# Kernel optimization log

Hardware: AMD Instinct MI355X
Metric: run time of the kernel (lower is better)

## Reference

```python
import jax, jax.numpy as jnp
import numpy as np
import math

# dims
B, L, D = 2, 2048, 1024          # batch, seq len, embedding_dim
HID, ATT, H = 1024, 512, 8       # linear_hidden_dim, attention_dim, num_heads
DQK, DUV = ATT // H, HID // H    # 64, 128
NBUCK = 64                       # time_num_buckets
MAX_SPAN = 86400 * 90            # max_time_span
EPS = 1e-6
OUT_DIM = 2 * HID + 2 * ATT      # uvqk output dim = 3072


def _time_boundaries():
    # RelativeAttentionBiasModule._build_boundaries: pure log buckets
    steps = NBUCK - 1
    log_part = np.exp(np.linspace(0.0, math.log(MAX_SPAN), steps))
    b = np.unique(np.floor(np.clip(log_part, 1, None)).astype(np.int64)).astype(np.float32)
    return jnp.asarray(b)

_BOUNDARIES = _time_boundaries()  # len <= 63, indices < NBUCK


def setup_inputs() -> dict:
    key = jax.random.key(0)
    ks = jax.random.split(key, 8)
    x = jax.random.normal(ks[0], (B, L, D), dtype=jnp.float32)
    timestamps = jnp.sort(
        jax.random.randint(ks[1], (B, L), 0, 2592000), axis=-1
    )  # chronological event times (seconds)
    attn_mask = jnp.tril(jnp.ones((L, L), dtype=bool))[None].repeat(B, axis=0)  # causal
    W_uvqk = jax.random.normal(ks[2], (OUT_DIM, D), dtype=jnp.float32) * 0.02
    b_uvqk = jnp.zeros((OUT_DIM,), dtype=jnp.float32)
    time_bias = jax.random.normal(ks[3], (NBUCK, H), dtype=jnp.float32) * 0.02
    W_o = jax.random.normal(ks[4], (D, HID), dtype=jnp.float32) * 0.02
    b_o = jnp.zeros((D,), dtype=jnp.float32)
    rms_w = jnp.ones((HID,), dtype=jnp.float32)
    return {"x": x, "timestamps": timestamps, "attn_mask": attn_mask,
            "W_uvqk": W_uvqk, "b_uvqk": b_uvqk, "time_bias": time_bias,
            "W_o": W_o, "b_o": b_o, "rms_w": rms_w}


def reference(x, timestamps, attn_mask, W_uvqk, b_uvqk, time_bias, W_o, b_o, rms_w):
    Bx, Lx, _ = x.shape
    scale = 1.0 / math.sqrt(DQK)

    # fused uvqk projection + act1 (silu)
    h = jax.nn.silu(x @ W_uvqk.T + b_uvqk)  # [B, L, OUT_DIM]
    u, v, q, k = jnp.split(h, [HID, 2 * HID, 2 * HID + ATT], axis=-1)

    def heads(t, d):  # [B, L, H*d] -> [B, H, L, d]
        return t.reshape(Bx, Lx, H, d).transpose(0, 2, 1, 3)

    u = heads(u, DUV)
    v = heads(v, DUV)
    q = heads(q, DQK) * scale
    k = heads(k, DQK)

    logits = jnp.einsum('bhid,bhjd->bhij', q.astype(jnp.float32), k.astype(jnp.float32))

    # bucketized relative-time bias (per-head)
    tdiff = jnp.abs(timestamps[:, :, None] - timestamps[:, None, :])
    tdiff = jnp.clip(tdiff, 1, None).astype(jnp.float32)  # clamp_min(1)
    bk = jnp.searchsorted(_BOUNDARIES, tdiff, side='left')  # torch.bucketize right=False
    rab = time_bias[bk].transpose(0, 3, 1, 2)  # [B, H, L, L]

    # pointwise silu attention (no softmax), masked
    A = jax.nn.silu(logits + rab) * attn_mask[:, None].astype(jnp.float32)

    y = jnp.einsum('bhij,bhjd->bhid', A, v)               # [B, H, L, DUV]
    y = y.transpose(0, 2, 1, 3).reshape(Bx, Lx, HID)       # merge heads
    u_m = u.transpose(0, 2, 1, 3).reshape(Bx, Lx, HID)

    # RMSNorm then U-gate
    rms = y * jax.lax.rsqrt(jnp.mean(y * y, axis=-1, keepdims=True) + EPS) * rms_w
    y_point = rms.astype(x.dtype) * u_m

    return y_point @ W_o.T + b_o  # [B, L, D]
```

## Files before the change

### kernel.cpp

```cpp
#include <hip/hip_runtime.h>
#include <hip/hip_bf16.h>

typedef float f32x4 __attribute__((ext_vector_type(4)));
typedef short s16x8 __attribute__((ext_vector_type(8)));
typedef short s16x4 __attribute__((ext_vector_type(4)));
typedef unsigned short u16x4 __attribute__((ext_vector_type(4)));

__device__ __forceinline__ float bf2f(unsigned short u) {
    union { unsigned int i; float f; } x; x.i = ((unsigned int)u) << 16; return x.f;
}
__device__ __forceinline__ unsigned short f2bf(float f) {
    union { float f; unsigned int i; } x; x.f = f;
    unsigned int r = x.i + 0x7FFFu + ((x.i >> 16) & 1u);
    return (unsigned short)(r >> 16);
}
__device__ __forceinline__ float silu(float v) {
    return v / (1.f + __expf(-v));
}

#define GLDS16(gp, lp) __builtin_amdgcn_global_load_lds( \
    (const __attribute__((address_space(1))) unsigned int*)(gp), \
    (__attribute__((address_space(3))) unsigned int*)(lp), 16, 0, 0)

__global__ __launch_bounds__(256) void cvt_bf16(
    const float* __restrict__ X, const float* __restrict__ W,
    const float* __restrict__ Wo,
    unsigned short* __restrict__ Xb, unsigned short* __restrict__ Wb,
    unsigned short* __restrict__ Wob)
{
    int idx = blockIdx.x * 256 + threadIdx.x;
    const float* src; unsigned short* dst; int off;
    if (idx < 1048576)       { src = X;  dst = Xb;  off = idx; }
    else if (idx < 1835008)  { src = W;  dst = Wb;  off = idx - 1048576; }
    else                     { src = Wo; dst = Wob; off = idx - 1835008; }
    f32x4 v = *reinterpret_cast<const f32x4*>(&src[(size_t)off * 4]);
    u16x4 o;
    #pragma unroll
    for (int j = 0; j < 4; ++j) o[j] = f2bf(v[j]);
    *reinterpret_cast<u16x4*>(&dst[(size_t)off * 4]) = o;
}

__global__ __launch_bounds__(256) void bucketize(
    const int* __restrict__ TS, unsigned char* __restrict__ BK)
{
    const int jt = blockIdx.x, it = blockIdx.y, b = blockIdx.z;
    if (jt > it) return;
    __shared__ int bndRaw[63];
    __shared__ int bnd[64];
    __shared__ int tsi[64], tsj[64];
    const int tid = threadIdx.x;
    if (tid < 63) {
        double step = log(7776000.0) / 62.0;
        double v = exp(step * (double)tid);
        if (v < 1.0) v = 1.0;
        bndRaw[tid] = (int)floor(v);
    }
    if (tid >= 64 && tid < 128) tsi[tid - 64] = TS[b * 2048 + it * 64 + (tid - 64)];
    else if (tid >= 128 && tid < 192) tsj[tid - 128] = TS[b * 2048 + jt * 64 + (tid - 128)];
    __syncthreads();
    if (tid == 0) {
        int c = 0, p = -1;
        for (int i = 0; i < 63; ++i) { int x = bndRaw[i]; if (x != p) { bnd[c++] = x; p = x; } }
        for (; c < 64; ++c) bnd[c] = 0x7FFFFFFF;
    }
    __syncthreads();
    const int il = tid & 63, jc = (tid >> 6) * 16;
    const int tiv = tsi[il];
    unsigned char out[16];
    #pragma unroll
    for (int u = 0; u < 16; ++u) {
        int td = tiv - tsj[jc + u]; td = td < 0 ? -td : td; if (td < 1) td = 1;
        int pos = 0;
        #pragma unroll
        for (int st = 32; st; st >>= 1)
            if (bnd[pos + st - 1] < td) pos += st;
        out[u] = (unsigned char)pos;
    }
    *reinterpret_cast<int4*>(&BK[((size_t)b << 22) + (size_t)(it * 64 + il) * 2048 + jt * 64 + jc]) =
        *reinterpret_cast<const int4*>(out);
}

__global__ __launch_bounds__(256) void gemm_uvqk(
    const unsigned short* __restrict__ Xb, const unsigned short* __restrict__ Wb,
    const float* __restrict__ bias,
    unsigned short* __restrict__ U, unsigned short* __restrict__ Vt,
    unsigned short* __restrict__ Q, unsigned short* __restrict__ K)
{
    __shared__ unsigned short sA[128][32];
    __shared__ unsigned short sB[128][32];
    const int tid = threadIdx.x;
    const int wv = tid >> 6, lane = tid & 63;
    const int g = lane >> 4, lr = lane & 15;
    const int wid = (blockIdx.x & 7) * 96 + (blockIdx.x >> 3);
    const int m0 = (wid & 31) * 128, n0 = (wid >> 5) * 128;
    const int wr = (wv >> 1) * 64, wc = (wv & 1) * 64;
    const int srow = (lane >> 2), scol = (lane & 3) * 8;
    f32x4 acc[4][4] = {};

    for (int k0 = 0; k0 < 1024; k0 += 32) {
        #pragma unroll
        for (int c = 0; c < 2; ++c) {
            int rb = (wv * 2 + c) * 16;
            GLDS16(&Xb[(size_t)(m0 + rb + srow) * 1024 + k0 + scol], &sA[rb][0]);
            GLDS16(&Wb[(size_t)(n0 + rb + srow) * 1024 + k0 + scol], &sB[rb][0]);
        }
        __syncthreads();
        s16x8 afr[4], bfr[4];
        #pragma unroll
        for (int i = 0; i < 4; ++i)
            afr[i] = *reinterpret_cast<const s16x8*>(&sA[wr + i * 16 + lr][g * 8]);
        #pragma unroll
        for (int i = 0; i < 4; ++i)
            bfr[i] = *reinterpret_cast<const s16x8*>(&sB[wc + i * 16 + lr][g * 8]);
        #pragma unroll
        for (int mi = 0; mi < 4; ++mi)
            #pragma unroll
            for (int ni = 0; ni < 4; ++ni)
                acc[mi][ni] = __builtin_amdgcn_mfma_f32_16x16x32_bf16(
                    afr[mi], bfr[ni], acc[mi][ni], 0, 0, 0);
        __syncthreads();
    }

    #pragma unroll
    for (int ni = 0; ni < 4; ++ni) {
        int n = n0 + wc + ni * 16 + lr;
        float bn = bias[n];
        #pragma unroll
        for (int mi = 0; mi < 4; ++mi) {
            #pragma unroll
            for (int r = 0; r < 4; ++r) {
                int m = m0 + wr + mi * 16 + g * 4 + r;
                float v = silu(acc[mi][ni][r] + bn);
                int b = m >> 11, l = m & 2047;
                if (n < 1024) {
                    U[(size_t)m * 1024 + n] = f2bf(v);
                } else if (n < 2048) {
                    int dd = n - 1024, h = dd >> 7, d = dd & 127;
                    Vt[(((size_t)(b * 8 + h) * 128 + d) << 11) + l] = f2bf(v);
                } else if (n < 2560) {
                    int dd = n - 2048, h = dd >> 6, d = dd & 63;
                    Q[((((size_t)(b * 8 + h) << 11) + l) << 6) + d] = f2bf(v * 0.125f);
                } else {
                    int dd = n - 2560, h = dd >> 6, d = dd & 63;
                    K[((((size_t)(b * 8 + h) << 11) + l) << 6) + d] = f2bf(v);
                }
            }
        }
    }
}

__global__ __launch_bounds__(256) void attn(
    const unsigned short* __restrict__ Q, const unsigned short* __restrict__ K,
    const unsigned short* __restrict__ Vt, const unsigned char* __restrict__ BK,
    const float* __restrict__ TB, float* __restrict__ Y)
{
    __shared__ __align__(16) unsigned short sK[2][64][64];
    __shared__ __align__(16) unsigned short sV[2][128][64];
    __shared__ __align__(16) unsigned char  sBK[2][64][64];
    __shared__ float tb[64];

    const int tid = threadIdx.x, wv = tid >> 6, lane = tid & 63;
    const int g = lane >> 4, lr = lane & 15;

    const int bid = blockIdx.x;
    const int xcd = bid & 7, slot = bid >> 3;
    const int s = slot & 31, p = s & 1, idx = s >> 1;
    const int bh = xcd * 2 + p;
    const int ti = (slot >= 32) ? (31 - idx) : idx;
    const int b = bh >> 3, h = bh & 7;
    const int i0 = ti * 64;
    const int irow = i0 + wv * 16;

    if (tid < 64) tb[tid] = TB[tid * 8 + h];

    const unsigned short* qb = Q + ((size_t)bh << 11) * 64;
    const unsigned short* kb = K + ((size_t)bh << 11) * 64;
    const unsigned short* vtb = Vt + ((size_t)bh << 7) * 2048;
    const unsigned char* bkb = BK + ((size_t)b << 22) + (size_t)i0 * 2048;

    s16x8 aq[2];
    #pragma unroll
    for (int kk = 0; kk < 2; ++kk)
        aq[kk] = *reinterpret_cast<const s16x8*>(&qb[(size_t)(irow + lr) * 64 + kk * 32 + g * 8]);

    auto stage = [&](int jt, int bsel) {
        const int j0 = jt * 64;
        #pragma unroll
        for (int c = 0; c < 2; ++c) {
            int id = c * 256 + tid;
            int row = id >> 3, c8 = id & 7;
            GLDS16(&kb[(size_t)(j0 + row) * 64 + ((c8 ^ (row & 7)) * 8)], &sK[bsel][row][c8 * 8]);
        }
        #pragma unroll
        for (int c = 0; c < 4; ++c) {
            int id = c * 256 + tid;
            int d = id >> 3, c8 = id & 7;
            GLDS16(&vtb[(size_t)d * 2048 + j0 + ((c8 ^ (d & 7)) * 8)], &sV[bsel][d][c8 * 8]);
        }
        {
            int row = tid >> 2, c16 = tid & 3;
            GLDS16(&bkb[(size_t)row * 2048 + j0 + ((c16 ^ (row & 3)) * 16)], &sBK[bsel][row][c16 * 16]);
        }
    };

    __syncthreads();
    stage(0, 0);

    f32x4 accy[8] = {};
    const int cs = lr & 7;
    const int r3 = lr & 3;
    const int ib = irow + lr;

    for (int jt = 0; jt <= ti; ++jt) {
        const int buf = jt & 1;
        __builtin_amdgcn_s_barrier();
        if (jt < ti) {
            stage(jt + 1, buf ^ 1);
            asm volatile("s_waitcnt vmcnt(7)" ::: "memory");
        } else {
            asm volatile("s_waitcnt vmcnt(0)" ::: "memory");
        }
        __builtin_amdgcn_s_barrier();

        const int j0 = jt * 64;
        f32x4 sacc[4] = {};
        unsigned int bw[4];
        #pragma unroll
        for (int ni = 0; ni < 4; ++ni) {
            bw[ni] = *reinterpret_cast<const unsigned int*>(
                &sBK[buf][wv * 16 + lr][0] + (((ni ^ r3) * 16) + g * 4));
            const int jl = ni * 16 + lr;
            #pragma unroll
            for (int kk = 0; kk < 2; ++kk) {
                s16x8 kf = *reinterpret_cast<const s16x8*>(
                    (const char*)&sK[buf][0][0] + jl * 128 + (((kk * 4 + g) ^ cs) << 4));
                sacc[ni] = __builtin_amdgcn_mfma_f32_16x16x32_bf16(kf, aq[kk], sacc[ni], 0, 0, 0);
            }
        }
        s16x4 pf[4];
        #pragma unroll
        for (int ni = 0; ni < 4; ++ni) {
            float pv0, pv1, pv2, pv3;
            {
                float v0 = silu(sacc[ni][0] + tb[bw[ni] & 255]);
                float v1 = silu(sacc[ni][1] + tb[(bw[ni] >> 8) & 255]);
                float v2 = silu(sacc[ni][2] + tb[(bw[ni] >> 16) & 255]);
                float v3 = silu(sacc[ni][3] + tb[(bw[ni] >> 24) & 255]);
                int jbase = j0 + ni * 16 + g * 4;
                pv0 = (jbase + 0 > ib) ? 0.f : v0;
                pv1 = (jbase + 1 > ib) ? 0.f : v1;
                pv2 = (jbase + 2 > ib) ? 0.f : v2;
                pv3 = (jbase + 3 > ib) ? 0.f : v3;
            }
            unsigned int w0, w1;
            asm("v_cvt_pk_bf16_f32 %0, %1, %2" : "=v"(w0) : "v"(pv0), "v"(pv1));
            asm("v_cvt_pk_bf16_f32 %0, %1, %2" : "=v"(w1) : "v"(pv2), "v"(pv3));
            union { unsigned int u[2]; s16x4 v; } cvt;
            cvt.u[0] = w0; cvt.u[1] = w1;
            pf[ni] = cvt.v;
        }
        #pragma unroll
        for (int di = 0; di < 8; ++di) {
            const int row = di * 16 + lr;
            #pragma unroll
            for (int ni = 0; ni < 4; ++ni) {
                s16x4 vf = *reinterpret_cast<const s16x4*>(
                    (const char*)&sV[buf][0][0] + row * 128 +
                    (((2 * ni + (g >> 1)) ^ cs) << 4) + ((g & 1) << 3));
                accy[di] = __builtin_amdgcn_mfma_f32_16x16x16bf16_1k(pf[ni], vf, accy[di], 0, 0, 0);
            }
        }
    }

    #pragma unroll
    for (int di = 0; di < 8; ++di)
        #pragma unroll
        for (int r = 0; r < 4; ++r) {
            int i = irow + g * 4 + r;
            Y[(size_t)((b << 11) + i) * 1024 + h * 128 + di * 16 + lr] = accy[di][r];
        }
}

__global__ __launch_bounds__(256) void rmsnorm_gate(
    const float* __restrict__ Y, const unsigned short* __restrict__ U,
    const float* __restrict__ rw, unsigned short* __restrict__ YP)
{
    __shared__ float red[4];
    const int row = blockIdx.x, tid = threadIdx.x;
    f32x4 v = *reinterpret_cast<const f32x4*>(&Y[(size_t)row * 1024 + tid * 4]);
    float ss = v[0] * v[0] + v[1] * v[1] + v[2] * v[2] + v[3] * v[3];
    #pragma unroll
    for (int off = 32; off; off >>= 1) ss += __shfl_down(ss, off);
    if ((tid & 63) == 0) red[tid >> 6] = ss;
    __syncthreads();
    float rms = rsqrtf((red[0] + red[1] + red[2] + red[3]) * (1.f / 1024.f) + 1e-6f);
    #pragma unroll
    for (int j = 0; j < 4; ++j) {
        int c = tid * 4 + j;
        float o = v[j] * rms * rw[c] * bf2f(U[(size_t)row * 1024 + c]);
        YP[(size_t)row * 1024 + c] = f2bf(o);
    }
}

__global__ __launch_bounds__(512) void gemm_out(
    const unsigned short* __restrict__ YP, const unsigned short* __restrict__ Wob,
    const float* __restrict__ bo, float* __restrict__ OUT)
{
    __shared__ unsigned short sA[128][32];
    __shared__ unsigned short sB[128][32];
    const int tid = threadIdx.x;
    const int wv = tid >> 6, lane = tid & 63;
    const int g = lane >> 4, lr = lane & 15;
    const int wid = (blockIdx.x & 7) * 32 + (blockIdx.x >> 3);
    const int m0 = (wid & 31) * 128, n0 = (wid >> 5) * 128;
    const int wr = (wv >> 2) * 64, wc = (wv & 3) * 32;
    f32x4 acc[4][2] = {};

    const int srow = tid >> 2, scol = (tid & 3) * 8;

    for (int k0 = 0; k0 < 1024; k0 += 32) {
        GLDS16(&YP[(size_t)(m0 + srow) * 1024 + k0 + scol], &sA[srow][scol]);
        GLDS16(&Wob[(size_t)(n0 + srow) * 1024 + k0 + scol], &sB[srow][scol]);
        __syncthreads();
        s16x8 afr[4], bfr[2];
        #pragma unroll
        for (int i = 0; i < 4; ++i)
            afr[i] = *reinterpret_cast<const s16x8*>(&sA[wr + i * 16 + lr][g * 8]);
        #pragma unroll
        for (int i = 0; i < 2; ++i)
            bfr[i] = *reinterpret_cast<const s16x8*>(&sB[wc + i * 16 + lr][g * 8]);
        #pragma unroll
        for (int mi = 0; mi < 4; ++mi)
            #pragma unroll
            for (int ni = 0; ni < 2; ++ni)
                acc[mi][ni] = __builtin_amdgcn_mfma_f32_16x16x32_bf16(
                    afr[mi], bfr[ni], acc[mi][ni], 0, 0, 0);
        __syncthreads();
    }

    #pragma unroll
    for (int ni = 0; ni < 2; ++ni) {
        int n = n0 + wc + ni * 16 + lr;
        float bn = bo[n];
        #pragma unroll
        for (int mi = 0; mi < 4; ++mi)
            #pragma unroll
            for (int r = 0; r < 4; ++r) {
                int m = m0 + wr + mi * 16 + g * 4 + r;
                OUT[(size_t)m * 1024 + n] = acc[mi][ni][r] + bn;
            }
    }
}

extern "C" void kernel_launch(void* const* d_in, const int* in_sizes, int n_in,
                              void* d_out, int out_size, void* d_ws, size_t ws_size,
                              hipStream_t stream) {
    const float* X     = (const float*)d_in[0];
    const int*   TS    = (const int*)d_in[1];
    const float* Wuvqk = (const float*)d_in[3];
    const float* buvqk = (const float*)d_in[4];
    const float* TB    = (const float*)d_in[5];
    const float* Wo    = (const float*)d_in[6];
    const float* bo    = (const float*)d_in[7];
    const float* rw    = (const float*)d_in[8];
    float* OUT = (float*)d_out;

    char* ws = (char*)d_ws;
    unsigned short* Qb  = (unsigned short*)(ws);
    unsigned short* Kb  = (unsigned short*)(ws + (4u << 20));
    unsigned short* Vt  = (unsigned short*)(ws + (8u << 20));
    unsigned short* Ub  = (unsigned short*)(ws + (16u << 20));
    float*          Yb  = (float*)(ws + (24u << 20));
    unsigned short* Xb  = (unsigned short*)(ws + (24u << 20));
    unsigned short* Wb  = (unsigned short*)(ws + (32u << 20));
    unsigned short* YP  = (unsigned short*)(ws + (40u << 20));
    unsigned char*  BKm = (unsigned char*)(ws + (48u << 20));
    unsigned short* Wob = (unsigned short*)(ws + (56u << 20));

    cvt_bf16<<<8192, 256, 0, stream>>>(X, Wuvqk, Wo, Xb, Wb, Wob);
    bucketize<<<dim3(32, 32, 2), 256, 0, stream>>>(TS, BKm);
    gemm_uvqk<<<768, 256, 0, stream>>>(Xb, Wb, buvqk, Ub, Vt, Qb, Kb);
    attn<<<512, 256, 0, stream>>>(Qb, Kb, Vt, BKm, TB, Yb);
    rmsnorm_gate<<<4096, 256, 0, stream>>>(Yb, Ub, rw, YP);
    gemm_out<<<256, 512, 0, stream>>>(YP, Wob, bo, OUT);
}
```

Before: 164.3 us.

## Load bucket indices directly to registers and unroll attention loop by two buffers

Drops the LDS staging of the bucket-index tile. Each lane now loads its four bias-index words straight from global memory into registers, double-buffered across iterations. The main loop is manually unrolled into two halves with fixed LDS buffer offsets, precomputed swizzled LDS addresses, a causal mask applied only on the diagonal tile, and a reciprocal-based silu. The goal is to cut LDS traffic, address arithmetic and per-element masking in the inner loop, at the cost of more registers and uncoalesced 4-byte global loads for the bias indices.

After: 167.9 us. +2.2%, slower.

```diff
diff --git a/kernel.cpp b/kernel.cpp
--- a/kernel.cpp
+++ b/kernel.cpp
@@ -16,6 +16,9 @@
 }
 __device__ __forceinline__ float silu(float v) {
     return v / (1.f + __expf(-v));
+}
+__device__ __forceinline__ float silu_fast(float v) {
+    return v * __builtin_amdgcn_rcpf(1.f + __expf(-v));
 }
 
 #define GLDS16(gp, lp) __builtin_amdgcn_global_load_lds( \
@@ -156,32 +159,44 @@
 {
     __shared__ __align__(16) unsigned short sK[2][64][64];
     __shared__ __align__(16) unsigned short sV[2][128][64];
-    __shared__ __align__(16) unsigned char  sBK[2][64][64];
     __shared__ float tb[64];
 
     const int tid = threadIdx.x, wv = tid >> 6, lane = tid & 63;
     const int g = lane >> 4, lr = lane & 15;
 
     const int bid = blockIdx.x;
-    const int xcd = bid & 7, slot = bid >> 3;
-    const int s = slot & 31, p = s & 1, idx = s >> 1;
-    const int bh = xcd * 2 + p;
-    const int ti = (slot >= 32) ? (31 - idx) : idx;
+    const int xcd = bid & 7, u = bid >> 3;
+    const int r_ = u >> 5, c_ = u & 31;
+    const int ti = r_ ? (31 - c_) : c_;
+    const int bh = xcd * 2 + r_;
     const int b = bh >> 3, h = bh & 7;
     const int i0 = ti * 64;
     const int irow = i0 + wv * 16;
 
     if (tid < 64) tb[tid] = TB[tid * 8 + h];
+    __syncthreads();
 
     const unsigned short* qb = Q + ((size_t)bh << 11) * 64;
     const unsigned short* kb = K + ((size_t)bh << 11) * 64;
     const unsigned short* vtb = Vt + ((size_t)bh << 7) * 2048;
-    const unsigned char* bkb = BK + ((size_t)b << 22) + (size_t)i0 * 2048;
+    const unsigned char* bkp = BK + ((size_t)b << 22) + (size_t)(irow + lr) * 2048 + g * 4;
 
     s16x8 aq[2];
     #pragma unroll
     for (int kk = 0; kk < 2; ++kk)
         aq[kk] = *reinterpret_cast<const s16x8*>(&qb[(size_t)(irow + lr) * 64 + kk * 32 + g * 8]);
+
+    const int cs = lr & 7;
+    const char* sKb = (const char*)&sK[0][0][0];
+    const char* sVb = (const char*)&sV[0][0][0];
+    int ka[2], va[4];
+    #pragma unroll
+    for (int kk = 0; kk < 2; ++kk)
+        ka[kk] = lr * 128 + (((kk * 4 + g) ^ cs) << 4);
+    #pragma unroll
+    for (int ni = 0; ni < 4; ++ni)
+        va[ni] = lr * 128 + (((2 * ni + (g >> 1)) ^ cs) << 4) + ((g & 1) << 3);
+    const int ib = irow + lr;
 
     auto stage = [&](int jt, int bsel) {
         const int j0 = jt * 64;
@@ -197,79 +212,89 @@
             int d = id >> 3, c8 = id & 7;
             GLDS16(&vtb[(size_t)d * 2048 + j0 + ((c8 ^ (d & 7)) * 8)], &sV[bsel][d][c8 * 8]);
         }
-        {
-            int row = tid >> 2, c16 = tid & 3;
-            GLDS16(&bkb[(size_t)row * 2048 + j0 + ((c16 ^ (row & 3)) * 16)], &sBK[bsel][row][c16 * 16]);
-        }
     };
 
-    __syncthreads();
+    unsigned int bwA[4], bwB[4];
+#define BIAS_LOAD(jt, bw) { const unsigned char* p_ = bkp + (size_t)(jt) * 64; \
+        bw[0] = *(const unsigned int*)(p_);      bw[1] = *(const unsigned int*)(p_ + 16); \
+        bw[2] = *(const unsigned int*)(p_ + 32); bw[3] = *(const unsigned int*)(p_ + 48); }
+
+    f32x4 accy[8] = {};
+
+#define COMPUTE(BUF, BW, jt) { \
+        const int j0 = (jt) * 64; \
+        f32x4 sacc[4] = {}; \
+        _Pragma("unroll") \
+        for (int ni = 0; ni < 4; ++ni) { \
+            _Pragma("unroll") \
+            for (int kk = 0; kk < 2; ++kk) { \
+                s16x8 kf = *reinterpret_cast<const s16x8*>(sKb + ka[kk] + ni * 2048 + (BUF) * 8192); \
+                sacc[ni] = __builtin_amdgcn_mfma_f32_16x16x32_bf16(kf, aq[kk], sacc[ni], 0, 0, 0); \
+            } \
+        } \
+        const bool diag = ((jt) == ti); \
+        s16x4 pf[4]; \
+        _Pragma("unroll") \
+        for (int ni = 0; ni < 4; ++ni) { \
+            float v0 = sacc[ni][0] + tb[BW[ni] & 255]; \
+            float v1 = sacc[ni][1] + tb[(BW[ni] >> 8) & 255]; \
+            float v2 = sacc[ni][2] + tb[(BW[ni] >> 16) & 255]; \
+            float v3 = sacc[ni][3] + tb[(BW[ni] >> 24) & 255]; \
+            v0 = silu_fast(v0); v1 = silu_fast(v1); v2 = silu_fast(v2); v3 = silu_fast(v3); \
+            if (diag) { \
+                int jb = j0 + ni * 16 + g * 4; \
+                if (jb + 0 > ib) v0 = 0.f; \
+                if (jb + 1 > ib) v1 = 0.f; \
+                if (jb + 2 > ib) v2 = 0.f; \
+                if (jb + 3 > ib) v3 = 0.f; \
+            } \
+            unsigned int w0, w1; \
+            asm("v_cvt_pk_bf16_f32 %0, %1, %2" : "=v"(w0) : "v"(v0), "v"(v1)); \
+            asm("v_cvt_pk_bf16_f32 %0, %1, %2" : "=v"(w1) : "v"(v2), "v"(v3)); \
+            union { unsigned int u_[2]; s16x4 v_; } cvt_; \
+            cvt_.u_[0] = w0; cvt_.u_[1] = w1; \
+            pf[ni] = cvt_.v_; \
+        } \
+        _Pragma("unroll") \
+        for (int di = 0; di < 8; ++di) { \
+            _Pragma("unroll") \
+            for (int ni = 0; ni < 4; ++ni) { \
+                s16x4 vf = *reinterpret_cast<const s16x4*>(sVb + va[ni] + di * 2048 + (BUF) * 16384); \
+                accy[di] = __builtin_amdgcn_mfma_f32_16x16x16bf16_1k(pf[ni], vf, accy[di], 0, 0, 0); \
+            } \
+        } }
+
     stage(0, 0);
-
-    f32x4 accy[8] = {};
-    const int cs = lr & 7;
-    const int r3 = lr & 3;
-    const int ib = irow + lr;
-
-    for (int jt = 0; jt <= ti; ++jt) {
-        const int buf = jt & 1;
+    BIAS_LOAD(0, bwA);
+
+    int jt = 0;
+    for (;;) {
+        __builtin_amdgcn_sched_barrier(0);
         __builtin_amdgcn_s_barrier();
-        if (jt < ti) {
-            stage(jt + 1, buf ^ 1);
-            asm volatile("s_waitcnt vmcnt(7)" ::: "memory");
+        if (jt + 1 <= ti) {
+            stage(jt + 1, 1);
+            BIAS_LOAD(jt + 1, bwB);
+            asm volatile("s_waitcnt vmcnt(10)" ::: "memory");
         } else {
             asm volatile("s_waitcnt vmcnt(0)" ::: "memory");
         }
         __builtin_amdgcn_s_barrier();
-
-        const int j0 = jt * 64;
-        f32x4 sacc[4] = {};
-        unsigned int bw[4];
-        #pragma unroll
-        for (int ni = 0; ni < 4; ++ni) {
-            bw[ni] = *reinterpret_cast<const unsigned int*>(
-                &sBK[buf][wv * 16 + lr][0] + (((ni ^ r3) * 16) + g * 4));
-            const int jl = ni * 16 + lr;
-            #pragma unroll
-            for (int kk = 0; kk < 2; ++kk) {
-                s16x8 kf = *reinterpret_cast<const s16x8*>(
-                    (const char*)&sK[buf][0][0] + jl * 128 + (((kk * 4 + g) ^ cs) << 4));
-                sacc[ni] = __builtin_amdgcn_mfma_f32_16x16x32_bf16(kf, aq[kk], sacc[ni], 0, 0, 0);
-            }
-        }
-        s16x4 pf[4];
-        #pragma unroll
-        for (int ni = 0; ni < 4; ++ni) {
-            float pv0, pv1, pv2, pv3;
-            {
-                float v0 = silu(sacc[ni][0] + tb[bw[ni] & 255]);
-                float v1 = silu(sacc[ni][1] + tb[(bw[ni] >> 8) & 255]);
-                float v2 = silu(sacc[ni][2] + tb[(bw[ni] >> 16) & 255]);
-                float v3 = silu(sacc[ni][3] + tb[(bw[ni] >> 24) & 255]);
-                int jbase = j0 + ni * 16 + g * 4;
-                pv0 = (jbase + 0 > ib) ? 0.f : v0;
-                pv1 = (jbase + 1 > ib) ? 0.f : v1;
-                pv2 = (jbase + 2 > ib) ? 0.f : v2;
-                pv3 = (jbase + 3 > ib) ? 0.f : v3;
-            }
-            unsigned int w0, w1;
-            asm("v_cvt_pk_bf16_f32 %0, %1, %2" : "=v"(w0) : "v"(pv0), "v"(pv1));
-            asm("v_cvt_pk_bf16_f32 %0, %1, %2" : "=v"(w1) : "v"(pv2), "v"(pv3));
-            union { unsigned int u[2]; s16x4 v; } cvt;
-            cvt.u[0] = w0; cvt.u[1] = w1;
-            pf[ni] = cvt.v;
-        }
-        #pragma unroll
-        for (int di = 0; di < 8; ++di) {
-            const int row = di * 16 + lr;
-            #pragma unroll
-            for (int ni = 0; ni < 4; ++ni) {
-                s16x4 vf = *reinterpret_cast<const s16x4*>(
-                    (const char*)&sV[buf][0][0] + row * 128 +
-                    (((2 * ni + (g >> 1)) ^ cs) << 4) + ((g & 1) << 3));
-                accy[di] = __builtin_amdgcn_mfma_f32_16x16x16bf16_1k(pf[ni], vf, accy[di], 0, 0, 0);
-            }
-        }
+        COMPUTE(0, bwA, jt);
+        if (jt + 1 > ti) break;
+        ++jt;
+        __builtin_amdgcn_sched_barrier(0);
+        __builtin_amdgcn_s_barrier();
+        if (jt + 1 <= ti) {
+            stage(jt + 1, 0);
+            BIAS_LOAD(jt + 1, bwA);
+            asm volatile("s_waitcnt vmcnt(10)" ::: "memory");
+        } else {
+            asm volatile("s_waitcnt vmcnt(0)" ::: "memory");
+        }
+        __builtin_amdgcn_s_barrier();
+        COMPUTE(1, bwB, jt);
+        if (jt + 1 > ti) break;
+        ++jt;
     }
 
     #pragma unroll
@@ -279,6 +304,8 @@
             int i = irow + g * 4 + r;
             Y[(size_t)((b << 11) + i) * 1024 + h * 128 + di * 16 + lr] = accy[di][r];
         }
+#undef COMPUTE
+#undef BIAS_LOAD
 }
 
 __global__ __launch_bounds__(256) void rmsnorm_gate(
```
